# Performance work log

Hardware: AMD Instinct MI355X
Metric: run time of the kernel (lower is better)

## Reference

```python
import jax, jax.numpy as jnp
import numpy as np

SR = 44100
DUR = 2.0
DS = 64
IN_GAIN = 10.0 ** (5.2 / 20.0)


def design_lr4_ir(freq, sr, n_taps=512):
    wc = np.tan(np.pi * freq / sr)
    wc2 = wc * wc
    root2 = np.sqrt(2.0)
    denom = 1 + root2 * wc + wc2
    b_lp = np.array([wc2 / denom, 2 * wc2 / denom, wc2 / denom])
    a_lp = np.array([1.0, 2 * (wc2 - 1) / denom, (1 - root2 * wc + wc2) / denom])
    b_hp = np.array([1 / denom, -2 / denom, 1 / denom])
    a_hp = np.array([1.0, 2 * (wc2 - 1) / denom, (1 - root2 * wc + wc2) / denom])
    b_lp4 = np.convolve(b_lp, b_lp); a_lp4 = np.convolve(a_lp, a_lp)
    b_hp4 = np.convolve(b_hp, b_hp); a_hp4 = np.convolve(a_hp, a_hp)
    def lfilter(b, a, x):
        y = np.zeros_like(x)
        for n in range(len(x)):
            acc = 0.0
            for i in range(len(b)):
                if n - i >= 0:
                    acc += b[i] * x[n - i]
            for i in range(1, len(a)):
                if n - i >= 0:
                    acc -= a[i] * y[n - i]
            y[n] = acc
        return y
    imp = np.zeros(n_taps); imp[0] = 1.0
    return lfilter(b_lp4, a_lp4, imp), lfilter(b_hp4, a_hp4, imp)


def _fir(x, w):
    # x: [B,C,T], w: flipped IR [K]; causal (left) padding, same filter per channel (grouped)
    K = w.shape[0]; C = x.shape[1]
    xp = jnp.pad(x, ((0, 0), (0, 0), (K - 1, 0)))
    kern = jnp.broadcast_to(w.reshape(1, 1, K), (C, 1, K))
    return jax.lax.conv_general_dilated(xp, kern, (1,), 'VALID',
                                        dimension_numbers=('NCH', 'OIH', 'NCH'),
                                        feature_group_count=C)


def _conv1d(x, w, b, pad, dil):
    y = jax.lax.conv_general_dilated(x, w, (1,), [(pad, pad)], rhs_dilation=(dil,),
                                     dimension_numbers=('NCH', 'OIH', 'NCH'))
    return y + b[None, :, None]


def _knee(x, thr, slope, k):
    diff = x - thr
    g_knee = slope * (diff + k / 2) ** 2 / (2 * k)
    return jnp.where(jnp.abs(diff) <= k / 2, g_knee,
                     jnp.where(diff > k / 2, slope * diff, jnp.zeros_like(x)))


def _forward(audio, params, rel_alphas, knee_db, ir_low_lp, ir_low_hp, ir_high_lp, ir_high_hp,
             w0, b0, w1, b1, w2, b2, w3, b3, w4, b4):
    batch, C, T = audio.shape
    audio_in = audio * IN_GAIN
    ott = params[:, -7:]
    amount = ott[:, 0][:, None, None]
    # 3-band LR4 crossover via 512-tap FIRs
    low = _fir(audio_in, ir_low_lp)
    m_h = _fir(audio_in, ir_low_hp)
    mid = _fir(m_h, ir_high_lp)
    high = _fir(m_h, ir_high_hp)
    bands = jnp.stack([high, mid, low], axis=1)            # [B,3,2,T]
    b_flat = bands.reshape(batch * 3, C, T)
    x_sq = jnp.mean(b_flat ** 2, axis=1, keepdims=True)    # [B3,1,T]
    Tc = T // DS
    x_rms = jnp.sqrt(x_sq[..., :Tc * DS].reshape(batch * 3, 1, Tc, DS).mean(-1) + 1e-7)
    # release-only envelope follower via cummax trick (faithful to torch code incl. repeat order)
    rel = jnp.repeat(rel_alphas, batch).reshape(-1, 1, 1)
    k = 1.0 - rel
    idx = jnp.arange(Tc, dtype=x_rms.dtype)
    kp = k ** idx
    ki = k ** (-idx)
    env_c = jax.lax.cummax(x_rms * ki, axis=2) * kp        # [B3,1,Tc]
    # linear interp back to T (align_corners=True)
    pos = jnp.arange(T, dtype=jnp.float32) * ((Tc - 1) / (T - 1))
    i0 = jnp.clip(jnp.floor(pos).astype(jnp.int32), 0, Tc - 2)
    frac = pos - i0.astype(jnp.float32)
    env = jnp.take(env_c, i0, axis=2) * (1 - frac) + jnp.take(env_c, i0 + 1, axis=2) * frac
    env_db = 20.0 * jnp.log10(env + 1e-7).reshape(batch, 3, T)
    t_a = jnp.stack([ott[:, 3], ott[:, 2], ott[:, 1]], axis=1)[..., None]
    t_b = jnp.stack([ott[:, 6], ott[:, 5], ott[:, 4]], axis=1)[..., None]
    above_slopes = jnp.array([1.0, 1.0 - 1 / 66.7, 1.0 - 1 / 66.7], jnp.float32).reshape(1, 3, 1)
    below_slope = jnp.float32(1.0 - 1.0 / 4.17)
    g_db = -_knee(env_db, t_a, above_slopes, knee_db) + _knee(-env_db, -t_b, below_slope, knee_db)
    out_gains = jnp.array([10.3, 5.7, 10.3], jnp.float32).reshape(1, 3, 1)
    total_g = 10.0 ** (jnp.clip(g_db + out_gains, -80.0, 40.0) / 20.0)
    combined = (bands * total_g[:, :, None, :]).sum(axis=1)  # [B,2,T]
    g = lambda z: jax.nn.gelu(z, approximate=False)
    r = g(_conv1d(combined, w0, b0, 1, 1))
    r = g(_conv1d(r, w1, b1, 2, 2))
    r = g(_conv1d(r, w2, b2, 4, 4))
    r = g(_conv1d(r, w3, b3, 8, 8))
    res = _conv1d(r, w4, b4, 1, 1)
    return (1.0 - amount) * audio + amount * (combined + res)


def setup_inputs() -> dict:
    B = 8
    T = int(SR * DUR)
    key = jax.random.key(0)
    ks = jax.random.split(key, 16)
    audio = jax.random.normal(ks[0], (B, 2, T), jnp.float32)
    amount = jax.random.uniform(ks[1], (B, 1), jnp.float32)
    thr = jax.random.uniform(ks[2], (B, 6), jnp.float32, minval=-40.0, maxval=0.0)
    params = jnp.concatenate([amount, thr], axis=1)
    ir_lp1, ir_hp1 = design_lr4_ir(88.3, SR)
    ir_lp2, ir_hp2 = design_lr4_ir(2500.0, SR)
    flip = lambda ir: jnp.asarray(ir[::-1].copy(), jnp.float32)
    sr_c = SR / DS
    rel_alphas = jnp.asarray(1.0 - np.exp(-1.0 / (sr_c * np.array([132.0, 282.0, 282.0]) / 1000.0)), jnp.float32)
    knee_db = jnp.float32(3.0)
    shapes = [(64, 2, 3), (64, 64, 3), (64, 64, 3), (64, 64, 3), (2, 64, 3)]
    out = {
        'audio': audio, 'params': params, 'rel_alphas': rel_alphas, 'knee_db': knee_db,
        'ir_low_lp': flip(ir_lp1), 'ir_low_hp': flip(ir_hp1),
        'ir_high_lp': flip(ir_lp2), 'ir_high_hp': flip(ir_hp2),
    }
    for i, (o, ci, kk) in enumerate(shapes):
        bound = 1.0 / np.sqrt(ci * kk)
        scale = 0.01 if i == len(shapes) - 1 else 1.0
        out[f'w{i}'] = jax.random.uniform(ks[4 + 2 * i], (o, ci, kk), jnp.float32, -bound, bound) * scale
        out[f'b{i}'] = jax.random.uniform(ks[5 + 2 * i], (o,), jnp.float32, -bound, bound) * scale
    return out


def reference(audio, params, rel_alphas, knee_db, ir_low_lp, ir_low_hp, ir_high_lp, ir_high_hp,
              w0, b0, w1, b1, w2, b2, w3, b3, w4, b4):
    return _forward(audio, params, rel_alphas, knee_db, ir_low_lp, ir_low_hp, ir_high_lp, ir_high_hp,
                    w0, b0, w1, b1, w2, b2, w3, b3, w4, b4)
```

## Files before the change

### kernel.cpp

```cpp
#include <hip/hip_runtime.h>
#include <math.h>

#define NT 88200
#define NB 8
#define TC 1378

static constexpr float IN_GAIN_F = 1.8197008586099834f;

#define OFF_A0    3072
#define OFF_A4    4096
#define OFF_ABF   5632
#define OFF_BANDS 24064
#define OFF_XRMS  4257664
#define OFF_ENV   4290736
#define OFF_WHL   4290736

typedef __attribute__((ext_vector_type(8))) short short8v;
typedef __attribute__((ext_vector_type(4))) short short4v;
typedef __attribute__((ext_vector_type(2))) unsigned int uint2v;
typedef __attribute__((ext_vector_type(4))) float float4v;
typedef __attribute__((ext_vector_type(16))) float float16v;
typedef __attribute__((ext_vector_type(8))) _Float16 half8v;

__device__ __forceinline__ float gelu_h(float x) {
  float s = __builtin_amdgcn_fmed3f(fmaf(0.28366667f, x, 0.5f), 0.f, 1.f);
  return x * s;
}
__device__ __forceinline__ short f2bf(float x) {
  unsigned int u = __float_as_uint(x);
  u += 0x7fffu + ((u >> 16) & 1u);
  return (short)(u >> 16);
}
__device__ __forceinline__ short f2fh(float x) {
  union { _Float16 h; short s; } u;
  u.h = (_Float16)x;
  return u.s;
}
__device__ __forceinline__ half8v s2h(short8v s) {
  union { short8v s; half8v h; } u;
  u.s = s;
  return u.h;
}
__device__ __forceinline__ unsigned int cvt_pk_bf16(float lo, float hi) {
  unsigned int d;
  asm("v_cvt_pk_bf16_f32 %0, %1, %2" : "=v"(d) : "v"(lo), "v"(hi));
  return d;
}

__global__ __launch_bounds__(256) void k_prep(
    const float* __restrict__ irLL, const float* __restrict__ irLH,
    const float* __restrict__ irHL, const float* __restrict__ irHH,
    const float* __restrict__ w0, const float* __restrict__ w1,
    const float* __restrict__ w2, const float* __restrict__ w3,
    const float* __restrict__ w4, float* __restrict__ ws)
{
  int gid = blockIdx.x * 256 + threadIdx.x;
  int task = blockIdx.y;
  if (task == 0) {
    short* whl = (short*)(ws + OFF_WHL);
    if (gid < 3072) {
      int band = gid >> 10, j = gid & 1023;
      float v = 0.f;
      if (j < 1023) {
        if (band == 2) {
          v = (j >= 511) ? irLL[j - 511] : 0.f;
        } else {
          const float* wb = (band == 0) ? irHH : irHL;
          int lo = j - 511; if (lo < 0) lo = 0;
          int hi = (j < 511) ? j : 511;
          float acc = 0.f;
          for (int i = lo; i <= hi; ++i) acc += irLH[i] * wb[j - i];
          v = acc;
        }
      }
      whl[band * 1152 + 64 + j] = f2fh(v);
    } else if (gid < 4608) {
      int z = gid - 3072;
      int entry;
      if (z < 384) {
        int band = z >> 7, r = z & 127;
        entry = band * 1152 + (r < 64 ? r : 1024 + r);
      } else {
        entry = 3 * 1152 + (z - 384);
      }
      whl[entry] = 0;
    }
  } else if (task == 1) {
    if (gid >= 2048) return;
    int wq = gid >> 9;
    int lane = (gid >> 3) & 63;
    int j = gid & 7;
    int l16 = lane & 15, q = lane >> 4;
    int m = wq * 16 + l16;
    int K = q * 8 + j;
    float val = (K < 6) ? w0[(m * 2 + (K & 1)) * 3 + (K >> 1)] : 0.f;
    ((short*)(ws + OFF_A0))[gid] = f2bf(val);
  } else if (task == 2) {
    if (gid >= 3072) return;
    int s = gid >> 9;
    int lane = (gid - s * 512) >> 3;
    int j = gid & 7;
    int m = lane & 15, q = lane >> 4;
    int K = s * 32 + q * 8 + j;
    int k = K >> 6, ic = K & 63;
    float val = (m < 2) ? w4[(m * 64 + ic) * 3 + k] : 0.f;
    ((short*)(ws + OFF_A4))[gid] = f2bf(val);
  } else if (task == 6) {
    for (int r = 0; r < 3; ++r) {
      int i = gid * 3 + r;
      if (i < 24 * TC) ws[OFF_XRMS + i] = 0.f;
    }
  } else {
    int l = task - 3;
    if (gid >= 12288) return;
    const float* wl = (l == 0) ? w1 : (l == 1) ? w2 : w3;
    int ocg = gid / 6144;
    int rem = gid - ocg * 6144;
    int s = rem / 512;
    int rem2 = rem - s * 512;
    int lane = rem2 >> 3;
    int j = gid & 7;
    int m = ocg * 32 + (lane & 31);
    int k = s * 16 + ((lane >> 5) << 3) + j;
    int tap = k >> 6, ic = k & 63;
    short* ap = (short*)(ws + OFF_ABF);
    ap[l * 12288 + gid] = f2bf(wl[(m * 64 + ic) * 3 + tap]);
  }
}

#define FT 320
__global__ __launch_bounds__(256) void k_firm(const float* __restrict__ audio,
                                              float* __restrict__ ws)
{
  __shared__ short xh[4][1360];
  __shared__ __align__(16) short wt[4608];
  __shared__ float ssum[3][5];
  int bc = blockIdx.x, tile = blockIdx.y;
  int t0b = tile * FT;
  int tid = threadIdx.x;
  if (tid < 15) ssum[tid / 5][tid % 5] = 0.f;
  const uint4* wsrc = (const uint4*)((const short*)(ws + OFF_WHL));
  uint4* wdst = (uint4*)wt;
  for (int i = tid; i < 576; i += 256) wdst[i] = wsrc[i];
  const float* x = audio + bc * NT;
  for (int i = tid; i < 1363; i += 256) {
    int g = t0b - 1022 + i;
    float v = (g >= 0 && g < NT) ? x[g] * IN_GAIN_F : 0.f;
    short h = f2fh(v);
#pragma unroll
    for (int c = 0; c < 4; ++c) {
      int idx = i - c;
      if (idx >= 0 && idx < 1360) xh[c][idx] = h;
    }
  }
  __syncthreads();

  int wave = tid >> 6, lane = tid & 63;
  int q = lane >> 4, l16 = lane & 15;
  int band = (l16 >= 10) ? 2 : (l16 >= 5 ? 1 : 0);
  if (l16 == 15) band = 3;
  int u = l16 - band * 5;
  const short* pAh = wt + band * 1152 + 64 + q * 8 - u * 16;
  int c = l16 & 3;
  int xoff = wave * 80 + q * 8 + ((l16 >> 2) << 2);
  const short* pBh = &xh[c][xoff];
  float4v a0 = {0.f, 0.f, 0.f, 0.f};
  float4v a1 = {0.f, 0.f, 0.f, 0.f};
#pragma unroll 2
  for (int s = 0; s < 34; s += 2) {
    half8v ah0 = *(const half8v*)(pAh + 32 * s);
    half8v ah1 = *(const half8v*)(pAh + 32 * (s + 1));
    short4v b00 = *(const short4v*)(pBh + 32 * s);
    short4v b01 = *(const short4v*)(pBh + 32 * s + 4);
    short4v b10 = *(const short4v*)(pBh + 32 * (s + 1));
    short4v b11 = *(const short4v*)(pBh + 32 * (s + 1) + 4);
    short8v bh0 = __builtin_shufflevector(b00, b01, 0, 1, 2, 3, 4, 5, 6, 7);
    short8v bh1 = __builtin_shufflevector(b10, b11, 0, 1, 2, 3, 4, 5, 6, 7);
    a0 = __builtin_amdgcn_mfma_f32_16x16x32_f16(ah0, s2h(bh0), a0, 0, 0, 0);
    a1 = __builtin_amdgcn_mfma_f32_16x16x32_f16(ah1, s2h(bh1), a1, 0, 0, 0);
  }
  float acc[4];
#pragma unroll
  for (int r = 0; r < 4; ++r) acc[r] = a0[r] + a1[r];

  int b = bc >> 1, ch = bc & 1;
  float* bands = ws + OFF_BANDS;
#pragma unroll
  for (int r = 0; r < 4; ++r) {
    int m = q * 4 + r;
    if (m < 15) {
      int bnd = (m >= 10) ? 2 : (m >= 5 ? 1 : 0);
      int uu = m - bnd * 5;
      int t = t0b + wave * 80 + uu * 16 + l16;
      if (t < NT) bands[((b * 3 + bnd) * 2 + ch) * NT + t] = acc[r];
    }
  }

  float s2[4];
#pragma unroll
  for (int r = 0; r < 4; ++r) {
    int m = q * 4 + r;
    s2[r] = (m < 15) ? acc[r] * acc[r] : 0.f;
  }
#pragma unroll
  for (int mask = 1; mask < 16; mask <<= 1)
#pragma unroll
    for (int r = 0; r < 4; ++r)
      s2[r] += __shfl_xor(s2[r], mask, 16);
  if (l16 == 0) {
#pragma unroll
    for (int r = 0; r < 4; ++r) {
      int m = q * 4 + r;
      if (m < 15) {
        int bnd = (m >= 10) ? 2 : (m >= 5 ? 1 : 0);
        int uu = m - bnd * 5;
        int jloc = (wave * 80 + uu * 16) >> 6;
        atomicAdd(&ssum[bnd][jloc], s2[r]);
      }
    }
  }
  __syncthreads();
  if (tid < 15) {
    int bnd = tid / 5, jl = tid - bnd * 5;
    int jg = tile * 5 + jl;
    if (jg < TC) atomicAdd(&ws[OFF_XRMS + (b * 3 + bnd) * TC + jg], ssum[bnd][jl]);
  }
}

__global__ __launch_bounds__(256) void k_scan(const float* __restrict__ rel_alphas,
                                              float* __restrict__ ws)
{
  __shared__ float pA[256], pB[256];
  int row = blockIdx.x;
  int tid = threadIdx.x;
  float kdec = 1.f - rel_alphas[row >> 3];
  const float* xr = ws + OFF_XRMS + row * TC;
  float v[6];
  int base = tid * 6;
#pragma unroll
  for (int s = 0; s < 6; ++s) {
    int j = base + s;
    v[s] = (j < TC) ? sqrtf(xr[j] * (0.5f / 64.f) + 1e-7f) : 0.f;
  }
  float r = v[0];
#pragma unroll
  for (int s = 1; s < 6; ++s) r = fmaxf(v[s], r * kdec);
  pA[tid] = r;
  __syncthreads();
  float k2 = kdec * kdec, k3 = k2 * kdec;
  float kp = k3 * k3;
  float* in = pA; float* outp = pB;
  for (int off = 1; off < 256; off <<= 1) {
    float val = in[tid];
    if (tid >= off) val = fmaxf(val, in[tid - off] * kp);
    outp[tid] = val;
    kp *= kp;
    __syncthreads();
    float* tmp = in; in = outp; outp = tmp;
  }
  float* env = ws + OFF_ENV + row * TC;
  float rr;
  if (tid > 0) {
    float carry = in[tid - 1];
    rr = fmaxf(v[0], carry * kdec);
  } else {
    rr = v[0];
  }
  if (base < TC) env[base] = rr;
#pragma unroll
  for (int s = 1; s < 6; ++s) {
    rr = fmaxf(v[s], rr * kdec);
    if (base + s < TC) env[base + s] = rr;
  }
}

#define PITCH 72
#define SPAN 256
#define TILE 224

__device__ __forceinline__ void mfma_layer32(const short* in, short* outb,
    const short* __restrict__ apk, const float* __restrict__ bias,
    const int d, int t0, int ocg, int posg, int lane)
{
  int l32 = lane & 31, hi = lane >> 5;
  float16v acc;
#pragma unroll
  for (int g = 0; g < 4; ++g) {
    float4 bv = *(const float4*)&bias[ocg * 32 + hi * 4 + g * 8];
    acc[4 * g + 0] = bv.x; acc[4 * g + 1] = bv.y;
    acc[4 * g + 2] = bv.z; acc[4 * g + 3] = bv.w;
  }
  int rbase = posg * 32 + l32;
  int rlo = rbase - d; rlo = rlo < 0 ? 0 : rlo;
  int rhi = rbase + d; rhi = rhi > SPAN - 1 ? SPAN - 1 : rhi;
  const short* pLo  = in + rlo * PITCH + hi * 8;
  const short* pMid = in + rbase * PITCH + hi * 8;
  const short* pHi  = in + rhi * PITCH + hi * 8;
  const short* ap = apk + (ocg * 12 * 64 + lane) * 8;

  short8v af[6];
#pragma unroll
  for (int k = 0; k < 6; ++k) af[k] = *(const short8v*)(ap + k * 512);
#pragma unroll
  for (int s = 0; s < 6; ++s) {
    const short* p = (s < 4) ? pLo : pMid;
    short8v bf = *(const short8v*)(p + (s & 3) * 16);
    acc = __builtin_amdgcn_mfma_f32_32x32x16_bf16(af[s], bf, acc, 0, 0, 0);
  }
#pragma unroll
  for (int k = 0; k < 6; ++k) af[k] = *(const short8v*)(ap + (k + 6) * 512);
#pragma unroll
  for (int s = 6; s < 12; ++s) {
    const short* p = (s < 8) ? pMid : pHi;
    short8v bf = *(const short8v*)(p + (s & 3) * 16);
    acc = __builtin_amdgcn_mfma_f32_32x32x16_bf16(af[s - 6], bf, acc, 0, 0, 0);
  }

  int t = t0 - 16 + rbase;
  bool z = (t < 0) | (t >= NT);
  short* wp = outb + rbase * PITCH + ocg * 32 + hi * 4;
#pragma unroll
  for (int g = 0; g < 4; ++g) {
    uint2v r;
    r[0] = cvt_pk_bf16(gelu_h(acc[4 * g + 0]), gelu_h(acc[4 * g + 1]));
    r[1] = cvt_pk_bf16(gelu_h(acc[4 * g + 2]), gelu_h(acc[4 * g + 3]));
    r[0] = z ? 0u : r[0];
    r[1] = z ? 0u : r[1];
    *(uint2v*)(wp + g * 8) = r;
  }
}

__global__ __launch_bounds__(1024, 8) void k_convnet(
    const float* __restrict__ audio, const float* __restrict__ params,
    const float* __restrict__ kneep,
    const float* __restrict__ b0, const float* __restrict__ b1,
    const float* __restrict__ b2, const float* __restrict__ b3,
    const float* __restrict__ b4, const float* __restrict__ ws,
    float* __restrict__ out)
{
  __shared__ float cmb[2][SPAN];
  __shared__ __align__(16) char ubuf[SPAN * 8 * 2];
  __shared__ __align__(16) short actA[SPAN * PITCH];
  __shared__ __align__(16) short actB[SPAN * PITCH];
  short (*bfL0)[8] = (short(*)[8])ubuf;
  int tile = blockIdx.x, b = blockIdx.y;
  int t0 = tile * TILE;
  int tid = threadIdx.x;
  int wave = tid >> 6, lane = tid & 63;

  if (tid < 2 * SPAN) {
    int ch = tid >> 8;
    int pos = tid & (SPAN - 1);
    int t = t0 - 16 + pos;
    float cc = 0.f;
    if (t >= 0 && t < NT) {
      const float* env = ws + OFF_ENV;
      const float* bands = ws + OFF_BANDS;
      float knee = kneep[0];
      float halfk = 0.5f * knee;
      float inv2k = 1.f / (2.f * knee);
      const float scale = (float)(1377.0 / 88199.0);
      float pos_f = (float)t * scale;
      int i0 = (int)floorf(pos_f);
      i0 = i0 < 0 ? 0 : (i0 > TC - 2 ? TC - 2 : i0);
      float frac = pos_f - (float)i0;
      const int tacol[3] = {3, 2, 1};
      const int tbcol[3] = {6, 5, 4};
      const float asl[3] = {1.f, (float)(1.0 - 1.0 / 66.7), (float)(1.0 - 1.0 / 66.7)};
      const float bsl = (float)(1.0 - 1.0 / 4.17);
      const float og[3] = {10.3f, 5.7f, 10.3f};
#pragma unroll
      for (int band = 0; band < 3; ++band) {
        int row = b * 3 + band;
        float e = env[row * TC + i0] * (1.f - frac) + env[row * TC + i0 + 1] * frac;
        float edb = 6.0205999132796239f * __builtin_amdgcn_logf(e + 1e-7f);
        float ta = params[b * 7 + tacol[band]];
        float tb = params[b * 7 + tbcol[band]];
        float d1 = edb - ta;
        float gk1 = asl[band] * (d1 + halfk) * (d1 + halfk) * inv2k;
        float ka = (fabsf(d1) <= halfk) ? gk1 : (d1 > halfk ? asl[band] * d1 : 0.f);
        float d2 = tb - edb;
        float gk2 = bsl * (d2 + halfk) * (d2 + halfk) * inv2k;
        float kb = (fabsf(d2) <= halfk) ? gk2 : (d2 > halfk ? bsl * d2 : 0.f);
        float gdb = -ka + kb + og[band];
        gdb = fminf(fmaxf(gdb, -80.f), 40.f);
        float g = __builtin_amdgcn_exp2f(gdb * 0.16609640474436812f);
        cc += bands[(row * 2 + ch) * NT + t] * g;
      }
    }
    cmb[ch][pos] = cc;
  }
  __syncthreads();

  for (int i = tid; i < SPAN * 8; i += 1024) {
    int r = i >> 3, j = i & 7;
    short v = 0;
    if (j < 6) {
      int k = j >> 1, ic = j & 1;
      int src = r - 1 + k;
      if (src >= 0 && src < SPAN) v = f2bf(cmb[ic][src]);
    }
    bfL0[r][j] = v;
  }
  __syncthreads();

  int quad = lane >> 4, l16 = lane & 15;

  {
    int wq = wave & 3, half = wave >> 2;
    const short* ap0 = (const short*)(ws + OFF_A0);
    short8v a0 = *(const short8v*)&ap0[(wq * 64 + lane) * 8];
    float4 bv = *(const float4*)&b0[wq * 16 + quad * 4];
    float4v acc[4];
#pragma unroll
    for (int n = 0; n < 4; ++n) { acc[n][0] = bv.x; acc[n][1] = bv.y; acc[n][2] = bv.z; acc[n][3] = bv.w; }
    short8v zf = {0, 0, 0, 0, 0, 0, 0, 0};
#pragma unroll
    for (int n = 0; n < 4; ++n) {
      int row = (half * 4 + n) * 16 + l16;
      short8v bf = (quad == 0) ? *(const short8v*)&bfL0[row][0] : zf;
      acc[n] = __builtin_amdgcn_mfma_f32_16x16x32_bf16(a0, bf, acc[n], 0, 0, 0);
    }
    int ocb = wq * 16 + quad * 4;
#pragma unroll
    for (int n = 0; n < 4; ++n) {
      int p = (half * 4 + n) * 16 + l16;
      int t = t0 - 16 + p;
      bool z = (t < 0) | (t >= NT);
      uint2v r;
      r[0] = cvt_pk_bf16(gelu_h(acc[n][0]), gelu_h(acc[n][1]));
      r[1] = cvt_pk_bf16(gelu_h(acc[n][2]), gelu_h(acc[n][3]));
      r[0] = z ? 0u : r[0];
      r[1] = z ? 0u : r[1];
      *(uint2v*)&actA[p * PITCH + ocb] = r;
    }
  }
  __syncthreads();

  int ocg = wave & 1, posg = wave >> 1;
  const short* apk = (const short*)(ws + OFF_ABF);
  mfma_layer32(actA, actB, apk,          b1, 2, t0, ocg, posg, lane);
  __syncthreads();
  mfma_layer32(actB, actA, apk + 12288,  b2, 4, t0, ocg, posg, lane);
  __syncthreads();
  mfma_layer32(actA, actB, apk + 24576,  b3, 8, t0, ocg, posg, lane);
  __syncthreads();

  if (wave < 14) {
    const short* ap4 = (const short*)(ws + OFF_A4);
    short8v a4f[6];
#pragma unroll
    for (int s = 0; s < 6; ++s) a4f[s] = *(const short8v*)&ap4[(s * 64 + lane) * 8];
    float4v acc = {0.f, 0.f, 0.f, 0.f};
    if (quad == 0) { acc[0] = b4[0]; acc[1] = b4[1]; }
#pragma unroll
    for (int s = 0; s < 6; ++s) {
      int kt = s >> 1;
      int ic0 = (s & 1) * 32 + quad * 8;
      int row = 16 + wave * 16 + l16 + kt - 1;
      short8v bf = *(const short8v*)&actB[row * PITCH + ic0];
      acc = __builtin_amdgcn_mfma_f32_16x16x32_bf16(a4f[s], bf, acc, 0, 0, 0);
    }
    if (quad == 0) {
      int t = t0 + wave * 16 + l16;
      if (t < NT) {
        float amt = params[b * 7];
#pragma unroll
        for (int r = 0; r < 2; ++r) {
          float aud = audio[(b * 2 + r) * NT + t];
          out[(b * 2 + r) * NT + t] =
              (1.f - amt) * aud + amt * (cmb[r][16 + wave * 16 + l16] + acc[r]);
        }
      }
    }
  }
}

extern "C" void kernel_launch(void* const* d_in, const int* in_sizes, int n_in,
                              void* d_out, int out_size, void* d_ws, size_t ws_size,
                              hipStream_t stream)
{
  (void)in_sizes; (void)n_in; (void)out_size; (void)ws_size;
  const float* audio = (const float*)d_in[0];
  const float* params = (const float*)d_in[1];
  const float* rel   = (const float*)d_in[2];
  const float* knee  = (const float*)d_in[3];
  const float* irLL  = (const float*)d_in[4];
  const float* irLH  = (const float*)d_in[5];
  const float* irHL  = (const float*)d_in[6];
  const float* irHH  = (const float*)d_in[7];
  const float* w0 = (const float*)d_in[8];  const float* b0 = (const float*)d_in[9];
  const float* w1 = (const float*)d_in[10]; const float* b1 = (const float*)d_in[11];
  const float* w2 = (const float*)d_in[12]; const float* b2 = (const float*)d_in[13];
  const float* w3 = (const float*)d_in[14]; const float* b3 = (const float*)d_in[15];
  const float* w4 = (const float*)d_in[16]; const float* b4 = (const float*)d_in[17];
  float* out = (float*)d_out;
  float* ws  = (float*)d_ws;

  hipLaunchKernelGGL(k_prep, dim3(48, 7), dim3(256), 0, stream,
                     irLL, irLH, irHL, irHH, w0, w1, w2, w3, w4, ws);
  hipLaunchKernelGGL(k_firm, dim3(16, 276), dim3(256), 0, stream, audio, ws);
  hipLaunchKernelGGL(k_scan, dim3(24), dim3(256), 0, stream, rel, ws);
  hipLaunchKernelGGL(k_convnet, dim3(394, 8), dim3(1024), 0, stream,
                     audio, params, knee, b0, b1, b2, b3, b4, ws, out);
}
```

Measured before the change: 271.4 us.

## Switch dilated conv layers from 32x32x16 to 16x16x32 MFMA tiling

The three middle dilated conv layers now use 16x16x32 bf16 MFMAs instead of 32x32x16. Each wave owns a 16-output-channel group and loops over four 16-position sub-tiles, reusing its six A fragments across them. The weight pre-pack layout is changed to match. This lowers accumulator register pressure (4 floats instead of 16) and may improve occupancy or scheduling, at the cost of more MFMA issues and more B-fragment loads from LDS. The last layer's weights are now loaded inside its loop instead of being preloaded into registers.

```diff
diff --git a/kernel.cpp b/kernel.cpp
--- a/kernel.cpp
+++ b/kernel.cpp
@@ -19,7 +19,6 @@
 typedef __attribute__((ext_vector_type(4))) short short4v;
 typedef __attribute__((ext_vector_type(2))) unsigned int uint2v;
 typedef __attribute__((ext_vector_type(4))) float float4v;
-typedef __attribute__((ext_vector_type(16))) float float16v;
 typedef __attribute__((ext_vector_type(8))) _Float16 half8v;
 
 __device__ __forceinline__ float gelu_h(float x) {
@@ -114,14 +113,14 @@
     int l = task - 3;
     if (gid >= 12288) return;
     const float* wl = (l == 0) ? w1 : (l == 1) ? w2 : w3;
-    int ocg = gid / 6144;
-    int rem = gid - ocg * 6144;
+    int g = gid / 3072;
+    int rem = gid - g * 3072;
     int s = rem / 512;
     int rem2 = rem - s * 512;
     int lane = rem2 >> 3;
     int j = gid & 7;
-    int m = ocg * 32 + (lane & 31);
-    int k = s * 16 + ((lane >> 5) << 3) + j;
+    int m = g * 16 + (lane & 15);
+    int k = s * 32 + ((lane >> 4) & 3) * 8 + j;
     int tap = k >> 6, ic = k & 63;
     short* ap = (short*)(ws + OFF_ABF);
     ap[l * 12288 + gid] = f2bf(wl[(m * 64 + ic) * 3 + tap]);
@@ -278,55 +277,39 @@
 #define SPAN 256
 #define TILE 224
 
-__device__ __forceinline__ void mfma_layer32(const short* in, short* outb,
+__device__ __forceinline__ void mfma_layer16(const short* in, short* outb,
     const short* __restrict__ apk, const float* __restrict__ bias,
-    const int d, int t0, int ocg, int posg, int lane)
-{
-  int l32 = lane & 31, hi = lane >> 5;
-  float16v acc;
-#pragma unroll
-  for (int g = 0; g < 4; ++g) {
-    float4 bv = *(const float4*)&bias[ocg * 32 + hi * 4 + g * 8];
-    acc[4 * g + 0] = bv.x; acc[4 * g + 1] = bv.y;
-    acc[4 * g + 2] = bv.z; acc[4 * g + 3] = bv.w;
-  }
-  int rbase = posg * 32 + l32;
-  int rlo = rbase - d; rlo = rlo < 0 ? 0 : rlo;
-  int rhi = rbase + d; rhi = rhi > SPAN - 1 ? SPAN - 1 : rhi;
-  const short* pLo  = in + rlo * PITCH + hi * 8;
-  const short* pMid = in + rbase * PITCH + hi * 8;
-  const short* pHi  = in + rhi * PITCH + hi * 8;
-  const short* ap = apk + (ocg * 12 * 64 + lane) * 8;
-
+    const int d, int t0, int g, int p, int lane)
+{
+  int l16 = lane & 15, l4 = (lane >> 4) & 3;
+  const short* ap = apk + g * 3072 + lane * 8;
   short8v af[6];
 #pragma unroll
-  for (int k = 0; k < 6; ++k) af[k] = *(const short8v*)(ap + k * 512);
-#pragma unroll
-  for (int s = 0; s < 6; ++s) {
-    const short* p = (s < 4) ? pLo : pMid;
-    short8v bf = *(const short8v*)(p + (s & 3) * 16);
-    acc = __builtin_amdgcn_mfma_f32_32x32x16_bf16(af[s], bf, acc, 0, 0, 0);
-  }
-#pragma unroll
-  for (int k = 0; k < 6; ++k) af[k] = *(const short8v*)(ap + (k + 6) * 512);
-#pragma unroll
-  for (int s = 6; s < 12; ++s) {
-    const short* p = (s < 8) ? pMid : pHi;
-    short8v bf = *(const short8v*)(p + (s & 3) * 16);
-    acc = __builtin_amdgcn_mfma_f32_32x32x16_bf16(af[s - 6], bf, acc, 0, 0, 0);
-  }
-
-  int t = t0 - 16 + rbase;
-  bool z = (t < 0) | (t >= NT);
-  short* wp = outb + rbase * PITCH + ocg * 32 + hi * 4;
-#pragma unroll
-  for (int g = 0; g < 4; ++g) {
+  for (int s = 0; s < 6; ++s) af[s] = *(const short8v*)(ap + s * 512);
+  float4 bv = *(const float4*)&bias[g * 16 + l4 * 4];
+#pragma unroll
+  for (int st = 0; st < 4; ++st) {
+    int pos = p * 64 + st * 16 + l16;
+    int rm = pos - d; rm = rm < 0 ? 0 : rm;
+    int rp = pos + d; rp = rp > SPAN - 1 ? SPAN - 1 : rp;
+    const short* pm = in + rm * PITCH + l4 * 8;
+    const short* p0 = in + pos * PITCH + l4 * 8;
+    const short* pp = in + rp * PITCH + l4 * 8;
+    float4v acc = {bv.x, bv.y, bv.z, bv.w};
+#pragma unroll
+    for (int s = 0; s < 6; ++s) {
+      const short* base = (s < 2) ? pm : (s < 4) ? p0 : pp;
+      short8v bf = *(const short8v*)(base + (s & 1) * 32);
+      acc = __builtin_amdgcn_mfma_f32_16x16x32_bf16(af[s], bf, acc, 0, 0, 0);
+    }
+    int t = t0 - 16 + pos;
+    bool z = (t < 0) | (t >= NT);
     uint2v r;
-    r[0] = cvt_pk_bf16(gelu_h(acc[4 * g + 0]), gelu_h(acc[4 * g + 1]));
-    r[1] = cvt_pk_bf16(gelu_h(acc[4 * g + 2]), gelu_h(acc[4 * g + 3]));
+    r[0] = cvt_pk_bf16(gelu_h(acc[0]), gelu_h(acc[1]));
+    r[1] = cvt_pk_bf16(gelu_h(acc[2]), gelu_h(acc[3]));
     r[0] = z ? 0u : r[0];
     r[1] = z ? 0u : r[1];
-    *(uint2v*)(wp + g * 8) = r;
+    *(uint2v*)(outb + pos * PITCH + g * 16 + l4 * 4) = r;
   }
 }
 
@@ -437,29 +420,27 @@
   }
   __syncthreads();
 
-  int ocg = wave & 1, posg = wave >> 1;
+  int g16 = wave & 3, p16 = wave >> 2;
   const short* apk = (const short*)(ws + OFF_ABF);
-  mfma_layer32(actA, actB, apk,          b1, 2, t0, ocg, posg, lane);
-  __syncthreads();
-  mfma_layer32(actB, actA, apk + 12288,  b2, 4, t0, ocg, posg, lane);
-  __syncthreads();
-  mfma_layer32(actA, actB, apk + 24576,  b3, 8, t0, ocg, posg, lane);
+  mfma_layer16(actA, actB, apk,          b1, 2, t0, g16, p16, lane);
+  __syncthreads();
+  mfma_layer16(actB, actA, apk + 12288,  b2, 4, t0, g16, p16, lane);
+  __syncthreads();
+  mfma_layer16(actA, actB, apk + 24576,  b3, 8, t0, g16, p16, lane);
   __syncthreads();
 
   if (wave < 14) {
     const short* ap4 = (const short*)(ws + OFF_A4);
-    short8v a4f[6];
-#pragma unroll
-    for (int s = 0; s < 6; ++s) a4f[s] = *(const short8v*)&ap4[(s * 64 + lane) * 8];
     float4v acc = {0.f, 0.f, 0.f, 0.f};
     if (quad == 0) { acc[0] = b4[0]; acc[1] = b4[1]; }
 #pragma unroll
     for (int s = 0; s < 6; ++s) {
+      short8v a4 = *(const short8v*)&ap4[(s * 64 + lane) * 8];
       int kt = s >> 1;
       int ic0 = (s & 1) * 32 + quad * 8;
       int row = 16 + wave * 16 + l16 + kt - 1;
       short8v bf = *(const short8v*)&actB[row * PITCH + ic0];
-      acc = __builtin_amdgcn_mfma_f32_16x16x32_bf16(a4f[s], bf, acc, 0, 0, 0);
+      acc = __builtin_amdgcn_mfma_f32_16x16x32_bf16(a4, bf, acc, 0, 0, 0);
     }
     if (quad == 0) {
       int t = t0 + wave * 16 + l16;
```

Result: faster. 257.2 us (-5.2%).
